# Optimization experiments

Measured on AMD Instinct MI355X. Metric: run time of the kernel, lower is better.

Reference implementation:

```python
import jax, jax.numpy as jnp
import numpy as np

B, T, L, H = 16, 16, 512, 768


def setup_inputs() -> dict:
    key = jax.random.key(0)
    k1, k2, k3, k4, k5, k6 = jax.random.split(key, 6)
    hn = jax.random.normal(k1, (B, L, H), dtype=jnp.float32)
    decoder_out = jax.random.normal(k2, (B, L, H), dtype=jnp.float32)
    W1 = jax.random.normal(k3, (H, H), dtype=jnp.float32) * (1.0 / np.sqrt(H))
    W2 = jax.random.normal(k4, (H, H), dtype=jnp.float32) * (1.0 / np.sqrt(H))
    V = jax.random.normal(k5, (H,), dtype=jnp.float32) * (1.0 / np.sqrt(H))
    # Ragged, consistent pointer indices: T monotone segment starts per sample,
    # gold boundary Yindex[b,t] in [Xindex[b,t], L).
    step = L // T  # 32
    Xindex = jnp.broadcast_to(jnp.arange(T, dtype=jnp.int64) * step, (B, T))
    offsets = jax.random.randint(k6, (B, T), 0, step, dtype=jnp.int64)
    Yindex = Xindex + offsets
    lens = jnp.full((B,), L, dtype=jnp.int64)
    return {"hn": hn, "decoder_out": decoder_out, "W1": W1, "W2": W2, "V": V,
            "Xindex": Xindex, "Yindex": Yindex, "lens": lens}


def reference(hn, decoder_out, W1, W2, V, Xindex, Yindex, lens):
    # Faithful batched form of training_decoder + pointerLayer:
    #   for each sample i, step j:
    #     en = hn[i, Xindex[i,j]:lens[i]]            (ragged suffix)
    #     dj = decoder_out[i, Yindex[i,j]]           (cur_dj = decoder_out[cur_groundy])
    #     s  = selu(V @ selu(W1 en + W2 dj))
    #     loss += NLL(log_softmax(s), Yindex[i,j]-Xindex[i,j])
    WE = jnp.einsum('blh,gh->blg', hn, W1)                        # [B,L,H]  nnW1(en)
    dj = jnp.take_along_axis(decoder_out, Yindex[:, :, None], axis=1)  # [B,T,H]
    WD = jnp.einsum('bth,gh->btg', dj, W2)                        # [B,T,H]  nnW2(dj)
    act = jax.nn.selu(WE[:, None, :, :] + WD[:, :, None, :])      # [B,T,L,H]
    scores = jax.nn.selu(jnp.einsum('btlh,h->btl', act, V))       # [B,T,L]
    pos = jnp.arange(hn.shape[1])
    mask = (pos[None, None, :] >= Xindex[:, :, None]) & (pos[None, None, :] < lens[:, None, None])
    neg_inf = jnp.finfo(scores.dtype).min
    masked = jnp.where(mask, scores, neg_inf)
    logp = masked - jax.scipy.special.logsumexp(masked, axis=-1, keepdims=True)
    # logits index (Yindex - Xindex) in the sliced array == global index Yindex
    gold = jnp.take_along_axis(logp, Yindex[:, :, None], axis=-1)[..., 0]  # [B,T]
    return -jnp.mean(gold)
```

## Files before the change

kernel.cpp:

```cpp
#include <hip/hip_runtime.h>
#include <hip/hip_bf16.h>
#include <math.h>

#define SELU_SCALE 1.0507009873554805f
#define SELU_ALPHA 1.6732632423543772f

static constexpr int B_ = 16, T_ = 16, L_ = 512, H_ = 768;

typedef __bf16 bf16x8 __attribute__((ext_vector_type(8)));
typedef __bf16 bf16x4 __attribute__((ext_vector_type(4)));
typedef float  f32x4  __attribute__((ext_vector_type(4)));

__device__ __forceinline__ float bf_lo(unsigned u) { return __uint_as_float(u << 16); }
__device__ __forceinline__ float bf_hi(unsigned u) { return __uint_as_float(u & 0xFFFF0000u); }

__device__ __forceinline__ float selu_core(float x) {
    float e = fmaf(__expf(x), SELU_ALPHA, -SELU_ALPHA);
    return x > 0.0f ? x : e;
}

__global__ __launch_bounds__(256) void cvt4_k(const float* __restrict__ in,
                                              __bf16* __restrict__ out, int n4) {
    int i = blockIdx.x * 256 + threadIdx.x;
    if (i < n4) {
        float4 f = ((const float4*)in)[i];
        bf16x4 o;
        o.x = (__bf16)f.x; o.y = (__bf16)f.y; o.z = (__bf16)f.z; o.w = (__bf16)f.w;
        ((bf16x4*)out)[i] = o;
    }
}

__global__ __launch_bounds__(256) void cvtW_k(const float* __restrict__ w1,
                                              const float* __restrict__ w2,
                                              __bf16* __restrict__ o1,
                                              __bf16* __restrict__ o2) {
    int i = blockIdx.x * 256 + threadIdx.x;
    const float* src = blockIdx.y ? w2 : w1;
    __bf16* dst = blockIdx.y ? o2 : o1;
    float4 f = ((const float4*)src)[i];
    bf16x4 o;
    o.x = (__bf16)f.x; o.y = (__bf16)f.y; o.z = (__bf16)f.z; o.w = (__bf16)f.w;
    ((bf16x4*)dst)[i] = o;
}

__global__ __launch_bounds__(192) void gather_dj_k(const float* __restrict__ dec,
                                                   const int* __restrict__ Yi,
                                                   __bf16* __restrict__ djb) {
    int bt = blockIdx.x;
    int b  = bt >> 4;
    int y  = Yi[bt];
    const float4* src = (const float4*)(dec + ((size_t)(b * L_ + y)) * H_);
    bf16x4* dst = (bf16x4*)(djb + (size_t)bt * H_);
    float4 f = src[threadIdx.x];
    bf16x4 o;
    o.x = (__bf16)f.x; o.y = (__bf16)f.y; o.z = (__bf16)f.z; o.w = (__bf16)f.w;
    dst[threadIdx.x] = o;
}

__device__ __forceinline__ void load16_lds(const __bf16* g, __bf16* l) {
    __builtin_amdgcn_global_load_lds(
        (const __attribute__((address_space(1))) unsigned int*)g,
        (__attribute__((address_space(3))) unsigned int*)l, 16, 0, 0);
}

__global__ __launch_bounds__(256) void gemm_nt_bf16_k(
        const __bf16* __restrict__ A, const __bf16* __restrict__ Bm,
        __bf16* __restrict__ C, int M, int N, int K) {
    __shared__ __bf16 As[128 * 32];
    __shared__ __bf16 Bs[128 * 32];
    const int wave = threadIdx.x >> 6;
    const int lane = threadIdx.x & 63;
    const int m0 = blockIdx.x * 128, n0 = blockIdx.y * 128;
    const int wm = (wave >> 1) * 64, wn = (wave & 1) * 64;
    const int lr = lane & 15, q = lane >> 4;

    const int srow = wave * 32 + (lane >> 2);
    const int scol = (lane & 3) * 8;
    const __bf16* Ag = A  + (size_t)(m0 + srow) * K + scol;
    const __bf16* Bg = Bm + (size_t)(n0 + srow) * K + scol;
    __bf16* Asw = &As[(wave * 32) * 32];
    __bf16* Bsw = &Bs[(wave * 32) * 32];

    f32x4 acc[4][4] = {};

    for (int k0 = 0; k0 < K; k0 += 32) {
        load16_lds(Ag + k0,            Asw);
        load16_lds(Ag + 16 * K + k0,   Asw + 16 * 32);
        load16_lds(Bg + k0,            Bsw);
        load16_lds(Bg + 16 * K + k0,   Bsw + 16 * 32);
        __syncthreads();
        bf16x8 af[4], bfr[4];
#pragma unroll
        for (int i = 0; i < 4; ++i)
            af[i] = *(const bf16x8*)&As[(wm + i * 16 + lr) * 32 + q * 8];
#pragma unroll
        for (int j = 0; j < 4; ++j)
            bfr[j] = *(const bf16x8*)&Bs[(wn + j * 16 + lr) * 32 + q * 8];
#pragma unroll
        for (int i = 0; i < 4; ++i)
#pragma unroll
            for (int j = 0; j < 4; ++j)
                acc[i][j] = __builtin_amdgcn_mfma_f32_16x16x32_bf16(af[i], bfr[j], acc[i][j], 0, 0, 0);
        __syncthreads();
    }

#pragma unroll
    for (int i = 0; i < 4; ++i)
#pragma unroll
        for (int j = 0; j < 4; ++j)
#pragma unroll
            for (int r = 0; r < 4; ++r) {
                int row = m0 + wm + i * 16 + q * 4 + r;
                int col = n0 + wn + j * 16 + lr;
                C[(size_t)row * N + col] = (__bf16)acc[i][j][r];
            }
}

__global__ __launch_bounds__(256) void scores_k(
        const __bf16* __restrict__ web, const __bf16* __restrict__ wdb,
        const float* __restrict__ V, const int* __restrict__ Xi,
        float* __restrict__ scores) {
    __shared__ float    we_s[16][772];
    __shared__ unsigned wd_s[16][388];

    const int b = blockIdx.x, l0 = blockIdx.y * 16;

    for (int c = threadIdx.x; c < 16 * 96; c += 256) {
        int r = c / 96, cc = c % 96;
        uint4 v = *(const uint4*)(web + ((size_t)(b * L_ + l0 + r)) * H_ + cc * 8);
        float4 f0, f1;
        f0.x = bf_lo(v.x); f0.y = bf_hi(v.x); f0.z = bf_lo(v.y); f0.w = bf_hi(v.y);
        f1.x = bf_lo(v.z); f1.y = bf_hi(v.z); f1.z = bf_lo(v.w); f1.w = bf_hi(v.w);
        *(float4*)&we_s[r][cc * 8]     = f0;
        *(float4*)&we_s[r][cc * 8 + 4] = f1;
    }
    for (int c = threadIdx.x; c < 16 * 96; c += 256) {
        int r = c / 96, cc = c % 96;
        *(uint4*)&wd_s[r][cc * 4] = *(const uint4*)(wdb + ((size_t)(b * T_ + r)) * H_ + cc * 8);
    }
    __syncthreads();

    const int t = threadIdx.x >> 4;
    const int ls = threadIdx.x & 15;
    const int l = l0 + ls;
    const int X = Xi[b * T_ + t];
    if (!__any(l >= X)) return;

    float a0 = 0.f, a1 = 0.f, a2 = 0.f, a3 = 0.f;
#pragma unroll 4
    for (int h = 0; h < H_; h += 8) {
        float4 w0 = *(const float4*)&we_s[ls][h];
        float4 w1 = *(const float4*)&we_s[ls][h + 4];
        uint4  wd = *(const uint4*)&wd_s[t][h >> 1];
        float4 v0 = *(const float4*)(V + h);
        float4 v1 = *(const float4*)(V + h + 4);
        a0 = fmaf(selu_core(w0.x + bf_lo(wd.x)), v0.x, a0);
        a1 = fmaf(selu_core(w0.y + bf_hi(wd.x)), v0.y, a1);
        a2 = fmaf(selu_core(w0.z + bf_lo(wd.y)), v0.z, a2);
        a3 = fmaf(selu_core(w0.w + bf_hi(wd.y)), v0.w, a3);
        a0 = fmaf(selu_core(w1.x + bf_lo(wd.z)), v1.x, a0);
        a1 = fmaf(selu_core(w1.y + bf_hi(wd.z)), v1.y, a1);
        a2 = fmaf(selu_core(w1.z + bf_lo(wd.w)), v1.z, a2);
        a3 = fmaf(selu_core(w1.w + bf_hi(wd.w)), v1.w, a3);
    }
    float dot = SELU_SCALE * ((a0 + a1) + (a2 + a3));
    float sc  = dot > 0.0f ? SELU_SCALE * dot
                           : SELU_SCALE * SELU_ALPHA * (__expf(dot) - 1.0f);
    scores[((size_t)(b * T_ + t)) * L_ + l] = sc;
}

__global__ __launch_bounds__(64) void nll_k(
        const float* __restrict__ scores, const int* __restrict__ Xi,
        const int* __restrict__ Yi, float* __restrict__ gold) {
    const int bt = blockIdx.x;
    const int lane = threadIdx.x;
    const int X = Xi[bt];
    const int Y = Yi[bt];
    const float* row = scores + (size_t)bt * L_;

    float m = -INFINITY;
    for (int l = X + lane; l < L_; l += 64) m = fmaxf(m, row[l]);
#pragma unroll
    for (int off = 32; off > 0; off >>= 1) m = fmaxf(m, __shfl_xor(m, off));

    float s = 0.0f;
    for (int l = X + lane; l < L_; l += 64) s += expf(row[l] - m);
#pragma unroll
    for (int off = 32; off > 0; off >>= 1) s += __shfl_xor(s, off);

    if (lane == 0) gold[bt] = row[Y] - m - logf(s);
}

__global__ __launch_bounds__(256) void finalize_k(const float* __restrict__ gold,
                                                  float* __restrict__ out) {
    __shared__ float red[4];
    const int lane = threadIdx.x & 63, wave = threadIdx.x >> 6;
    float v = gold[threadIdx.x];
#pragma unroll
    for (int off = 32; off > 0; off >>= 1) v += __shfl_xor(v, off);
    if (lane == 0) red[wave] = v;
    __syncthreads();
    if (threadIdx.x == 0) out[0] = -(red[0] + red[1] + red[2] + red[3]) * (1.0f / 256.0f);
}

extern "C" void kernel_launch(void* const* d_in, const int* in_sizes, int n_in,
                              void* d_out, int out_size, void* d_ws, size_t ws_size,
                              hipStream_t stream) {
    const float* hn  = (const float*)d_in[0];
    const float* dec = (const float*)d_in[1];
    const float* W1  = (const float*)d_in[2];
    const float* W2  = (const float*)d_in[3];
    const float* V   = (const float*)d_in[4];
    const int*   Xi  = (const int*)d_in[5];
    const int*   Yi  = (const int*)d_in[6];
    float* out = (float*)d_out;

    char* ws = (char*)d_ws;
    size_t off = 0;
    auto alloc = [&](size_t bytes) -> char* {
        char* p = ws + off;
        off += (bytes + 255) & ~(size_t)255;
        return p;
    };
    __bf16* hnb    = (__bf16*)alloc((size_t)B_ * L_ * H_ * 2);
    __bf16* w1b    = (__bf16*)alloc((size_t)H_ * H_ * 2);
    __bf16* w2b    = (__bf16*)alloc((size_t)H_ * H_ * 2);
    __bf16* djb    = (__bf16*)alloc((size_t)B_ * T_ * H_ * 2);
    __bf16* web    = (__bf16*)alloc((size_t)B_ * L_ * H_ * 2);
    __bf16* wdb    = (__bf16*)alloc((size_t)B_ * T_ * H_ * 2);
    float*  scores = (float*)alloc((size_t)B_ * T_ * L_ * 4);
    float*  gold   = (float*)alloc((size_t)B_ * T_ * 4);

    cvt4_k<<<(B_ * L_ * H_ / 4 + 255) / 256, 256, 0, stream>>>(hn, hnb, B_ * L_ * H_ / 4);
    cvtW_k<<<dim3(H_ * H_ / 4 / 256, 2), 256, 0, stream>>>(W1, W2, w1b, w2b);
    gather_dj_k<<<B_ * T_, 192, 0, stream>>>(dec, Yi, djb);

    gemm_nt_bf16_k<<<dim3(64, 6), 256, 0, stream>>>(hnb, w1b, web, B_ * L_, H_, H_);
    gemm_nt_bf16_k<<<dim3(2, 6), 256, 0, stream>>>(djb, w2b, wdb, B_ * T_, H_, H_);

    scores_k<<<dim3(B_, L_ / 16), 256, 0, stream>>>(web, wdb, V, Xi, scores);
    nll_k<<<B_ * T_, 64, 0, stream>>>(scores, Xi, Yi, gold);
    finalize_k<<<1, 256, 0, stream>>>(gold, out);
}
```

Before: 177.7 us.

## Fuse prep and GEMM launches, shrink GEMM tile, swizzle LDS, atomic loss reduction

New measurement: 161.7 us. 1.1x faster.

```diff
diff --git a/kernel.cpp b/kernel.cpp
--- a/kernel.cpp
+++ b/kernel.cpp
@@ -19,42 +19,38 @@
     return x > 0.0f ? x : e;
 }
 
-__global__ __launch_bounds__(256) void cvt4_k(const float* __restrict__ in,
-                                              __bf16* __restrict__ out, int n4) {
-    int i = blockIdx.x * 256 + threadIdx.x;
-    if (i < n4) {
-        float4 f = ((const float4*)in)[i];
-        bf16x4 o;
-        o.x = (__bf16)f.x; o.y = (__bf16)f.y; o.z = (__bf16)f.z; o.w = (__bf16)f.w;
-        ((bf16x4*)out)[i] = o;
-    }
-}
-
-__global__ __launch_bounds__(256) void cvtW_k(const float* __restrict__ w1,
-                                              const float* __restrict__ w2,
-                                              __bf16* __restrict__ o1,
-                                              __bf16* __restrict__ o2) {
-    int i = blockIdx.x * 256 + threadIdx.x;
-    const float* src = blockIdx.y ? w2 : w1;
-    __bf16* dst = blockIdx.y ? o2 : o1;
-    float4 f = ((const float4*)src)[i];
+__device__ __forceinline__ bf16x4 cvt4(float4 f) {
     bf16x4 o;
     o.x = (__bf16)f.x; o.y = (__bf16)f.y; o.z = (__bf16)f.z; o.w = (__bf16)f.w;
-    ((bf16x4*)dst)[i] = o;
-}
-
-__global__ __launch_bounds__(192) void gather_dj_k(const float* __restrict__ dec,
-                                                   const int* __restrict__ Yi,
-                                                   __bf16* __restrict__ djb) {
-    int bt = blockIdx.x;
-    int b  = bt >> 4;
-    int y  = Yi[bt];
-    const float4* src = (const float4*)(dec + ((size_t)(b * L_ + y)) * H_);
-    bf16x4* dst = (bf16x4*)(djb + (size_t)bt * H_);
-    float4 f = src[threadIdx.x];
-    bf16x4 o;
-    o.x = (__bf16)f.x; o.y = (__bf16)f.y; o.z = (__bf16)f.z; o.w = (__bf16)f.w;
-    dst[threadIdx.x] = o;
+    return o;
+}
+
+__global__ __launch_bounds__(256) void prep_k(
+        const float* __restrict__ hn, const float* __restrict__ w1,
+        const float* __restrict__ w2, const float* __restrict__ dec,
+        const int* __restrict__ Yi,
+        __bf16* __restrict__ hnb, __bf16* __restrict__ w1b,
+        __bf16* __restrict__ w2b, __bf16* __restrict__ djb) {
+    const int N0 = B_ * L_ * H_ / 4;
+    const int NW = H_ * H_ / 4;
+    const int N1 = N0 + NW, N2 = N1 + NW;
+    int i = blockIdx.x * 256 + threadIdx.x;
+    if (i < N0) {
+        ((bf16x4*)hnb)[i] = cvt4(((const float4*)hn)[i]);
+    } else if (i < N1) {
+        int j = i - N0;
+        ((bf16x4*)w1b)[j] = cvt4(((const float4*)w1)[j]);
+    } else if (i < N2) {
+        int j = i - N1;
+        ((bf16x4*)w2b)[j] = cvt4(((const float4*)w2)[j]);
+    } else {
+        int j = i - N2;
+        int bt = j / 192, c = j % 192;
+        int b = bt >> 4;
+        int y = Yi[bt];
+        ((bf16x4*)djb)[bt * 192 + c] =
+            cvt4(((const float4*)dec)[(b * L_ + y) * 192 + c]);
+    }
 }
 
 __device__ __forceinline__ void load16_lds(const __bf16* g, __bf16* l) {
@@ -62,42 +58,65 @@
         (const __attribute__((address_space(1))) unsigned int*)g,
         (__attribute__((address_space(3))) unsigned int*)l, 16, 0, 0);
 }
-
-__global__ __launch_bounds__(256) void gemm_nt_bf16_k(
-        const __bf16* __restrict__ A, const __bf16* __restrict__ Bm,
-        __bf16* __restrict__ C, int M, int N, int K) {
-    __shared__ __bf16 As[128 * 32];
+__device__ __forceinline__ int sw3(int row) { return (row ^ (row >> 2)) & 3; }
+
+__global__ __launch_bounds__(256) void gemm_k(
+        const __bf16* __restrict__ hnb, const __bf16* __restrict__ djb,
+        const __bf16* __restrict__ w1b, const __bf16* __restrict__ w2b,
+        __bf16* __restrict__ web, __bf16* __restrict__ wdb) {
+    __shared__ __bf16 As[64 * 32];
     __shared__ __bf16 Bs[128 * 32];
+
+    int bx = blockIdx.x;
+    const __bf16* A; const __bf16* Bw; __bf16* C;
+    if (bx < 768) { A = hnb; Bw = w1b; C = web; }
+    else          { bx -= 768; A = djb; Bw = w2b; C = wdb; }
+    const int m0 = (bx / 6) * 64, n0 = (bx % 6) * 128;
+
     const int wave = threadIdx.x >> 6;
     const int lane = threadIdx.x & 63;
-    const int m0 = blockIdx.x * 128, n0 = blockIdx.y * 128;
-    const int wm = (wave >> 1) * 64, wn = (wave & 1) * 64;
+    const int wm = (wave >> 1) * 32, wn = (wave & 1) * 64;
     const int lr = lane & 15, q = lane >> 4;
 
-    const int srow = wave * 32 + (lane >> 2);
-    const int scol = (lane & 3) * 8;
-    const __bf16* Ag = A  + (size_t)(m0 + srow) * K + scol;
-    const __bf16* Bg = Bm + (size_t)(n0 + srow) * K + scol;
-    __bf16* Asw = &As[(wave * 32) * 32];
-    __bf16* Bsw = &Bs[(wave * 32) * 32];
-
-    f32x4 acc[4][4] = {};
-
-    for (int k0 = 0; k0 < K; k0 += 32) {
-        load16_lds(Ag + k0,            Asw);
-        load16_lds(Ag + 16 * K + k0,   Asw + 16 * 32);
-        load16_lds(Bg + k0,            Bsw);
-        load16_lds(Bg + 16 * K + k0,   Bsw + 16 * 32);
+    const int arow = wave * 16 + (lane >> 2);
+    const int acol = ((lane & 3) ^ sw3(arow)) * 8;
+    const int brow0 = wave * 32 + (lane >> 2);
+    const int bcol0 = ((lane & 3) ^ sw3(brow0)) * 8;
+    const int brow1 = brow0 + 16;
+    const int bcol1 = ((lane & 3) ^ sw3(brow1)) * 8;
+    const __bf16* Ag  = A  + (size_t)(m0 + arow)  * 768 + acol;
+    const __bf16* Bg0 = Bw + (size_t)(n0 + brow0) * 768 + bcol0;
+    const __bf16* Bg1 = Bw + (size_t)(n0 + brow1) * 768 + bcol1;
+    __bf16* Asw = &As[wave * 16 * 32];
+    __bf16* Bsw0 = &Bs[wave * 32 * 32];
+    __bf16* Bsw1 = Bsw0 + 16 * 32;
+
+    int aoff[2], boff[4];
+#pragma unroll
+    for (int i = 0; i < 2; ++i) {
+        int r = wm + i * 16 + lr;
+        aoff[i] = r * 32 + ((q ^ sw3(r)) & 3) * 8;
+    }
+#pragma unroll
+    for (int j = 0; j < 4; ++j) {
+        int r = wn + j * 16 + lr;
+        boff[j] = r * 32 + ((q ^ sw3(r)) & 3) * 8;
+    }
+
+    f32x4 acc[2][4] = {};
+
+    for (int k0 = 0; k0 < 768; k0 += 32) {
+        load16_lds(Ag  + k0, Asw);
+        load16_lds(Bg0 + k0, Bsw0);
+        load16_lds(Bg1 + k0, Bsw1);
         __syncthreads();
-        bf16x8 af[4], bfr[4];
-#pragma unroll
-        for (int i = 0; i < 4; ++i)
-            af[i] = *(const bf16x8*)&As[(wm + i * 16 + lr) * 32 + q * 8];
-#pragma unroll
-        for (int j = 0; j < 4; ++j)
-            bfr[j] = *(const bf16x8*)&Bs[(wn + j * 16 + lr) * 32 + q * 8];
-#pragma unroll
-        for (int i = 0; i < 4; ++i)
+        bf16x8 af[2], bfr[4];
+#pragma unroll
+        for (int i = 0; i < 2; ++i) af[i]  = *(const bf16x8*)&As[aoff[i]];
+#pragma unroll
+        for (int j = 0; j < 4; ++j) bfr[j] = *(const bf16x8*)&Bs[boff[j]];
+#pragma unroll
+        for (int i = 0; i < 2; ++i)
 #pragma unroll
             for (int j = 0; j < 4; ++j)
                 acc[i][j] = __builtin_amdgcn_mfma_f32_16x16x32_bf16(af[i], bfr[j], acc[i][j], 0, 0, 0);
@@ -105,14 +124,14 @@
     }
 
 #pragma unroll
-    for (int i = 0; i < 4; ++i)
+    for (int i = 0; i < 2; ++i)
 #pragma unroll
         for (int j = 0; j < 4; ++j)
 #pragma unroll
             for (int r = 0; r < 4; ++r) {
                 int row = m0 + wm + i * 16 + q * 4 + r;
                 int col = n0 + wn + j * 16 + lr;
-                C[(size_t)row * N + col] = (__bf16)acc[i][j][r];
+                C[(size_t)row * 768 + col] = (__bf16)acc[i][j][r];
             }
 }
 
@@ -122,6 +141,7 @@
         float* __restrict__ scores) {
     __shared__ float    we_s[16][772];
     __shared__ unsigned wd_s[16][388];
+    __shared__ float    v_s[768];
 
     const int b = blockIdx.x, l0 = blockIdx.y * 16;
 
@@ -138,6 +158,7 @@
         int r = c / 96, cc = c % 96;
         *(uint4*)&wd_s[r][cc * 4] = *(const uint4*)(wdb + ((size_t)(b * T_ + r)) * H_ + cc * 8);
     }
+    if (threadIdx.x < 192) *(float4*)&v_s[threadIdx.x * 4] = ((const float4*)V)[threadIdx.x];
     __syncthreads();
 
     const int t = threadIdx.x >> 4;
@@ -152,8 +173,8 @@
         float4 w0 = *(const float4*)&we_s[ls][h];
         float4 w1 = *(const float4*)&we_s[ls][h + 4];
         uint4  wd = *(const uint4*)&wd_s[t][h >> 1];
-        float4 v0 = *(const float4*)(V + h);
-        float4 v1 = *(const float4*)(V + h + 4);
+        float4 v0 = *(const float4*)&v_s[h];
+        float4 v1 = *(const float4*)&v_s[h + 4];
         a0 = fmaf(selu_core(w0.x + bf_lo(wd.x)), v0.x, a0);
         a1 = fmaf(selu_core(w0.y + bf_hi(wd.x)), v0.y, a1);
         a2 = fmaf(selu_core(w0.z + bf_lo(wd.y)), v0.z, a2);
@@ -169,9 +190,9 @@
     scores[((size_t)(b * T_ + t)) * L_ + l] = sc;
 }
 
-__global__ __launch_bounds__(64) void nll_k(
+__global__ __launch_bounds__(64) void loss_k(
         const float* __restrict__ scores, const int* __restrict__ Xi,
-        const int* __restrict__ Yi, float* __restrict__ gold) {
+        const int* __restrict__ Yi, float* __restrict__ out) {
     const int bt = blockIdx.x;
     const int lane = threadIdx.x;
     const int X = Xi[bt];
@@ -188,19 +209,8 @@
 #pragma unroll
     for (int off = 32; off > 0; off >>= 1) s += __shfl_xor(s, off);
 
-    if (lane == 0) gold[bt] = row[Y] - m - logf(s);
-}
-
-__global__ __launch_bounds__(256) void finalize_k(const float* __restrict__ gold,
-                                                  float* __restrict__ out) {
-    __shared__ float red[4];
-    const int lane = threadIdx.x & 63, wave = threadIdx.x >> 6;
-    float v = gold[threadIdx.x];
-#pragma unroll
-    for (int off = 32; off > 0; off >>= 1) v += __shfl_xor(v, off);
-    if (lane == 0) red[wave] = v;
-    __syncthreads();
-    if (threadIdx.x == 0) out[0] = -(red[0] + red[1] + red[2] + red[3]) * (1.0f / 256.0f);
+    if (lane == 0)
+        atomicAdd(out, (m + logf(s) - row[Y]) * (1.0f / (B_ * T_)));
 }
 
 extern "C" void kernel_launch(void* const* d_in, const int* in_sizes, int n_in,
@@ -229,16 +239,13 @@
     __bf16* web    = (__bf16*)alloc((size_t)B_ * L_ * H_ * 2);
     __bf16* wdb    = (__bf16*)alloc((size_t)B_ * T_ * H_ * 2);
     float*  scores = (float*)alloc((size_t)B_ * T_ * L_ * 4);
-    float*  gold   = (float*)alloc((size_t)B_ * T_ * 4);
-
-    cvt4_k<<<(B_ * L_ * H_ / 4 + 255) / 256, 256, 0, stream>>>(hn, hnb, B_ * L_ * H_ / 4);
-    cvtW_k<<<dim3(H_ * H_ / 4 / 256, 2), 256, 0, stream>>>(W1, W2, w1b, w2b);
-    gather_dj_k<<<B_ * T_, 192, 0, stream>>>(dec, Yi, djb);
-
-    gemm_nt_bf16_k<<<dim3(64, 6), 256, 0, stream>>>(hnb, w1b, web, B_ * L_, H_, H_);
-    gemm_nt_bf16_k<<<dim3(2, 6), 256, 0, stream>>>(djb, w2b, wdb, B_ * T_, H_, H_);
+
+    hipMemsetAsync(out, 0, sizeof(float), stream);
+
+    prep_k<<<7488, 256, 0, stream>>>(hn, W1, W2, dec, Yi, hnb, w1b, w2b, djb);
+
+    gemm_k<<<792, 256, 0, stream>>>(hnb, djb, w1b, w2b, web, wdb);
 
     scores_k<<<dim3(B_, L_ / 16), 256, 0, stream>>>(web, wdb, V, Xi, scores);
-    nll_k<<<B_ * T_, 64, 0, stream>>>(scores, Xi, Yi, gold);
-    finalize_k<<<1, 256, 0, stream>>>(gold, out);
-}
+    loss_k<<<B_ * T_, 64, 0, stream>>>(scores, Xi, Yi, out);
+}
```
